# Kernel tuning notes

Measured on AMD Instinct MI355X. Metric: run time of the kernel, lower is better.

## Reference

```python
import jax, jax.numpy as jnp
import numpy as np

B, H, W, C = 4, 48, 48, 256
NUM_HEADS = 8
DEPTH = C // NUM_HEADS  # 32


def setup_inputs() -> dict:
    key = jax.random.key(0)
    ks = jax.random.split(key, 8)
    scale = 1.0 / np.sqrt(C)
    return {
        "inputs": jax.random.normal(ks[0], (B, H, W, C), dtype=jnp.float32),
        "wq": jax.random.normal(ks[1], (C, C), dtype=jnp.float32) * scale,
        "bq": jax.random.normal(ks[2], (C,), dtype=jnp.float32) * 0.01,
        "wk": jax.random.normal(ks[3], (C, C), dtype=jnp.float32) * scale,
        "bk": jax.random.normal(ks[4], (C,), dtype=jnp.float32) * 0.01,
        "wv": jax.random.normal(ks[5], (C, C), dtype=jnp.float32) * scale,
        "bv": jax.random.normal(ks[6], (C,), dtype=jnp.float32) * 0.01,
        "gamma": jax.random.normal(ks[7], (), dtype=jnp.float32) * 0.1,
    }


def reference(inputs, wq, bq, wk, bk, wv, bv, gamma):
    b, h, w, c = inputs.shape
    n = h * w  # number of tokens

    def proj_split(wm, bm):
        # 1x1 conv == per-pixel dense: [b,h,w,c] @ [c,c] + bias
        y = jnp.einsum('bhwc,cd->bhwd', inputs, wm) + bm
        # split heads -> [b, num_heads, n, depth]
        return y.reshape(b, n, NUM_HEADS, DEPTH).transpose(0, 2, 1, 3)

    q = proj_split(wq, bq) / jnp.sqrt(jnp.asarray(DEPTH, inputs.dtype))
    k = proj_split(wk, bk)
    v = proj_split(wv, bv)

    s = jnp.einsum('bnqd,bnkd->bnqk', q, k)        # [b, heads, n, n]
    a = jax.nn.softmax(s, axis=-1)
    o = jnp.einsum('bnqk,bnkd->bnqd', a, v)        # [b, heads, n, depth]
    o = o.transpose(0, 2, 1, 3).reshape(b, h, w, c)
    return gamma * o + inputs
```

## Files before the change

### kernel.cpp

```cpp
#include <hip/hip_runtime.h>
#include <hip/hip_bf16.h>
#include <cstdint>

#define B_    4
#define NH    8
#define N_TOK 2304
#define D_    32
#define C_    256
#define M_ROWS (B_ * N_TOK)
#define KVB   64
#define NT2   (N_TOK / KVB)
#define M_FIX 10.0f

typedef float  f32x4  __attribute__((ext_vector_type(4)));
typedef short  bf16x8 __attribute__((ext_vector_type(8)));

#define GLOADLDS(g, l) __builtin_amdgcn_global_load_lds( \
    (const __attribute__((address_space(1))) unsigned*)(g), \
    (__attribute__((address_space(3))) unsigned*)(l), 16, 0, 0)

static __device__ __forceinline__ unsigned short f2bf(float f) {
    union { float f; unsigned u; } v; v.f = f;
    unsigned u = v.u;
    u += 0x7FFF + ((u >> 16) & 1);
    return (unsigned short)(u >> 16);
}

static __device__ __forceinline__ unsigned cvt_pk_bf16(float a, float b) {
    unsigned r;
    asm("v_cvt_pk_bf16_f32 %0, %1, %2" : "=v"(r) : "v"(a), "v"(b));
    return r;
}

__global__ void k_prep(const float* __restrict__ x,
                       const float* __restrict__ w0, const float* __restrict__ w1,
                       const float* __restrict__ w2,
                       unsigned short* __restrict__ xb, unsigned short* __restrict__ wt) {
    __shared__ float tile[64][65];
    int bid = blockIdx.x;
    if (bid < 2304) {
        int i = bid * 256 + threadIdx.x;
        float4 v = reinterpret_cast<const float4*>(x)[i];
        ushort4 o;
        o.x = f2bf(v.x); o.y = f2bf(v.y); o.z = f2bf(v.z); o.w = f2bf(v.w);
        reinterpret_cast<ushort4*>(xb)[i] = o;
        return;
    }
    int t   = bid - 2304;
    int mat = t >> 4;  t &= 15;
    const float* w = (mat == 0) ? w0 : (mat == 1) ? w1 : w2;
    int tc  = (t & 3) * 64;
    int td  = (t >> 2) * 64;
    int tid = threadIdx.x;
    int r0  = tid >> 6;
    int x0  = tid & 63;
#pragma unroll
    for (int it = 0; it < 16; ++it) {
        int c = it * 4 + r0;
        tile[c][x0] = w[(tc + c) * C_ + td + x0];
    }
    __syncthreads();
    unsigned short* wto = wt + mat * (C_ * C_);
#pragma unroll
    for (int it = 0; it < 16; ++it) {
        int d = it * 4 + r0;
        wto[(td + d) * C_ + tc + x0] = f2bf(tile[x0][d]);
    }
}

__global__ __launch_bounds__(256) void k_proj(
    const unsigned short* __restrict__ xb,
    const unsigned short* __restrict__ wtb,
    const float* __restrict__ bq, const float* __restrict__ bk, const float* __restrict__ bv,
    unsigned short* __restrict__ qo, unsigned short* __restrict__ ko, unsigned short* __restrict__ vto)
{
    __shared__ __align__(16) unsigned short A_lds[3][64][32];
    __shared__ __align__(16) unsigned short B_lds[3][128][32];

    int rows0 = blockIdx.x * 64;
    int cols0 = blockIdx.y * 128;
    int mat   = cols0 >> 8;
    const float* bias = (mat == 0) ? bq : (mat == 1) ? bk : bv;
    float scale = (mat == 0) ? (0.17677669529663687f * 1.4426950408889634f) : 1.0f;

    int tid = threadIdx.x, wave = tid >> 6, lane = tid & 63;
    int lr = lane & 15, lg = lane >> 4;
    int wr = wave >> 1, wc = wave & 1;

    int srow = lane >> 2, sslot = lane & 3;
    int ra   = wave * 16 + srow;
    int keyA = ((ra >> 1) & 1) | (((ra >> 3) & 1) << 1);
    const unsigned short* asrc = xb + (rows0 + ra) * C_ + ((sslot ^ keyA) * 8);
    int rb   = wave * 32 + srow;
    int keyB0 = ((rb >> 1) & 1) | (((rb >> 3) & 1) << 1);
    int keyB1 = (((rb + 16) >> 1) & 1) | ((((rb + 16) >> 3) & 1) << 1);
    const unsigned short* bsrc0 = wtb + (cols0 + rb) * C_ + ((sslot ^ keyB0) * 8);
    const unsigned short* bsrc1 = wtb + (cols0 + rb + 16) * C_ + ((sslot ^ keyB1) * 8);

    char* aldsb = (char*)&A_lds[0][0][0];
    char* bldsb = (char*)&B_lds[0][0][0];
    int adst = wave * 1024;
    int bdst0 = wave * 2048, bdst1 = bdst0 + 1024;

    int xorb = (((lr >> 1) & 1) << 4) | (((lr >> 3) & 1) << 5);
    int fcol = (lg * 16) ^ xorb;
    int arow0 = wr * 32 + lr;
    int brow0 = wc * 64 + lr;

#define PSTAGE(ks, bidx) do {                               \
        int ko_ = (ks) * 32;                                \
        char* ad = aldsb + (bidx) * 4096;                   \
        char* bd = bldsb + (bidx) * 8192;                   \
        GLOADLDS(asrc + ko_, ad + adst);                    \
        GLOADLDS(bsrc0 + ko_, bd + bdst0);                  \
        GLOADLDS(bsrc1 + ko_, bd + bdst1);                  \
    } while (0)

    PSTAGE(0, 0);
    PSTAGE(1, 1);
    asm volatile("s_waitcnt vmcnt(3)" ::: "memory");
    __builtin_amdgcn_s_barrier();

    f32x4 acc[2][4];
#pragma unroll
    for (int i = 0; i < 2; ++i)
#pragma unroll
        for (int j = 0; j < 4; ++j) acc[i][j] = (f32x4){0.f, 0.f, 0.f, 0.f};

    int b0 = 0;
    for (int ks = 0; ks < 8; ++ks) {
        if (ks + 2 < 8) {
            int b2 = b0 + 2; if (b2 >= 3) b2 -= 3;
            PSTAGE(ks + 2, b2);
        }
        const char* ac = aldsb + b0 * 4096;
        const char* bc = bldsb + b0 * 8192;

        bf16x8 a[2], b[4];
#pragma unroll
        for (int fr = 0; fr < 2; ++fr)
            a[fr] = *reinterpret_cast<const bf16x8*>(ac + (arow0 + fr * 16) * 64 + fcol);
#pragma unroll
        for (int fn = 0; fn < 4; ++fn)
            b[fn] = *reinterpret_cast<const bf16x8*>(bc + (brow0 + fn * 16) * 64 + fcol);

        __builtin_amdgcn_s_setprio(1);
#pragma unroll
        for (int fr = 0; fr < 2; ++fr)
#pragma unroll
            for (int fn = 0; fn < 4; ++fn)
                acc[fr][fn] = __builtin_amdgcn_mfma_f32_16x16x32_bf16(a[fr], b[fn], acc[fr][fn], 0, 0, 0);
        __builtin_amdgcn_s_setprio(0);

        if (ks < 7) {
            if (ks + 2 < 8) asm volatile("s_waitcnt vmcnt(3)" ::: "memory");
            else            asm volatile("s_waitcnt vmcnt(0)" ::: "memory");
            __builtin_amdgcn_s_barrier();
        }
        b0 = (b0 + 1 == 3) ? 0 : b0 + 1;
    }
#undef PSTAGE

    int bidx = rows0 / N_TOK;
    int nb   = rows0 - bidx * N_TOK + wr * 32 + lg * 4;

    if (mat == 2) {
#pragma unroll
        for (int fr = 0; fr < 2; ++fr)
#pragma unroll
            for (int fn = 0; fn < 4; ++fn) {
                int cm = (cols0 & 255) + wc * 64 + fn * 16 + lr;
                float bsv = bias[cm];
                int hh = cm >> 5, d = cm & 31;
                uint2 pr;
                pr.x = cvt_pk_bf16(acc[fr][fn][0] + bsv, acc[fr][fn][1] + bsv);
                pr.y = cvt_pk_bf16(acc[fr][fn][2] + bsv, acc[fr][fn][3] + bsv);
                *reinterpret_cast<uint2*>(vto + ((bidx * NH + hh) * D_ + d) * N_TOK + nb + fr * 16) = pr;
            }
    } else {
        unsigned short* dst = (mat == 0) ? qo : ko;
#pragma unroll
        for (int fr = 0; fr < 2; ++fr)
#pragma unroll
            for (int fn = 0; fn < 4; ++fn) {
                int cm = (cols0 & 255) + wc * 64 + fn * 16 + lr;
                float bsv = bias[cm];
                int hh = cm >> 5, d = cm & 31;
#pragma unroll
                for (int j = 0; j < 4; ++j) {
                    float val = (acc[fr][fn][j] + bsv) * scale;
                    dst[((bidx * NH + hh) * N_TOK + nb + fr * 16 + j) * D_ + d] = f2bf(val);
                }
            }
    }
}

__global__ __launch_bounds__(256, 4) void k_attn(
    const unsigned short* __restrict__ qb,
    const unsigned short* __restrict__ kb,
    const unsigned short* __restrict__ vtg,
    const float* __restrict__ x,
    const float* __restrict__ gamma_p,
    float* __restrict__ out)
{
    __shared__ __align__(16) unsigned short K_lds[3][KVB][32];
    __shared__ __align__(16) unsigned short Vt_lds[3][32][KVB];

    int wid = (blockIdx.x & 7) * 72 + (blockIdx.x >> 3);
    int bh  = wid / 18;
    int qb0 = (wid % 18) * 128;

    int tid = threadIdx.x, wave = tid >> 6, lane = tid & 63;
    int lr = lane & 15, lg = lane >> 4;

    const unsigned short* Q  = qb  + bh * N_TOK * D_;
    const unsigned short* K  = kb  + bh * N_TOK * D_;
    const unsigned short* Vt = vtg + bh * D_ * N_TOK;

    int qrowA = qb0 + wave * 32 + lr;
    bf16x8 qA = *reinterpret_cast<const bf16x8*>(Q + qrowA * D_ + lg * 8);
    bf16x8 qB = *reinterpret_cast<const bf16x8*>(Q + (qrowA + 16) * D_ + lg * 8);

    bool stK = wave < 2;
    int kr0   = 32 * wave + (lane >> 2);
    int kslot = ((kr0 >> 1) & 1) | (((kr0 >> 3) & 1) << 1);
    int koff0 = kr0 * D_ + (((lane & 3) ^ kslot) * 8);
    int koff1 = koff0 + 16 * D_;
    int kdst0 = wave * 2048 + lane * 16;
    int kdst1 = kdst0 + 1024;
    int vw    = wave - 2;
    int vr0   = 16 * vw + (lane >> 3);
    int vkeyw = vr0 & 7;
    int voff0 = vr0 * N_TOK + (((lane & 7) ^ vkeyw) * 8);
    int voff1 = (vr0 + 8) * N_TOK + (((lane & 7) ^ vkeyw) * 8);
    int vdst0 = vw * 2048 + lane * 16;
    int vdst1 = vdst0 + 1024;

    char* kldsb = (char*)&K_lds[0][0][0];
    char* vldsb = (char*)&Vt_lds[0][0][0];

#define STAGE(st, bidx) do {                                    \
        if (stK) {                                              \
            const unsigned short* Kn = K + (st) * (KVB * D_);   \
            char* kd = kldsb + (bidx) * 4096;                   \
            GLOADLDS(Kn + koff0, kd + kdst0);                   \
            GLOADLDS(Kn + koff1, kd + kdst1);                   \
        } else {                                                \
            const unsigned short* Vn = Vt + (st) * KVB;         \
            char* vd = vldsb + (bidx) * 4096;                   \
            GLOADLDS(Vn + voff0, vd + vdst0);                   \
            GLOADLDS(Vn + voff1, vd + vdst1);                   \
        } } while (0)

    STAGE(0, 0);
    STAGE(1, 1);
    asm volatile("s_waitcnt vmcnt(2)" ::: "memory");
    __builtin_amdgcn_s_barrier();

    f32x4 accA0 = (f32x4){0.f, 0.f, 0.f, 0.f};
    f32x4 accA1 = (f32x4){0.f, 0.f, 0.f, 0.f};
    f32x4 accB0 = (f32x4){0.f, 0.f, 0.f, 0.f};
    f32x4 accB1 = (f32x4){0.f, 0.f, 0.f, 0.f};
    f32x4 acclA = (f32x4){0.f, 0.f, 0.f, 0.f};
    f32x4 acclB = (f32x4){0.f, 0.f, 0.f, 0.f};

    union { unsigned w[4]; bf16x8 v; } ones;
    ones.w[0] = 0x3F803F80u; ones.w[1] = 0x3F803F80u;
    ones.w[2] = 0x3F803F80u; ones.w[3] = 0x3F803F80u;

    int kread_key = (((lr >> 1) & 1) << 4) | (((lr >> 2) & 1) << 5);
    int krow_lane = (8 * (lr >> 2) + (lr & 3)) * 64 + ((lg * 16) ^ kread_key);
    int vkey = (lr & 7) << 4;

    const f32x4 zinit = (f32x4){-M_FIX, -M_FIX, -M_FIX, -M_FIX};

    int b0 = 0;
    for (int t = 0; t < NT2; ++t) {
        if (t + 2 < NT2) {
            int b2 = b0 + 2; if (b2 >= 3) b2 -= 3;
            STAGE(t + 2, b2);
        }
        const char* kc = kldsb + b0 * 4096;
        const char* vc = vldsb + b0 * 4096;

        f32x4 sA[4], sB[4];
        __builtin_amdgcn_s_setprio(1);
#pragma unroll
        for (int kt = 0; kt < 4; ++kt) {
            bf16x8 kf = *reinterpret_cast<const bf16x8*>(
                kc + (kt >> 1) * 2048 + (kt & 1) * 256 + krow_lane);
            sA[kt] = __builtin_amdgcn_mfma_f32_16x16x32_bf16(kf, qA, zinit, 0, 0, 0);
            sB[kt] = __builtin_amdgcn_mfma_f32_16x16x32_bf16(kf, qB, zinit, 0, 0, 0);
        }
        __builtin_amdgcn_s_setprio(0);

#pragma unroll
        for (int kseg = 0; kseg < 2; ++kseg) {
            union { unsigned w[4]; bf16x8 v; } paA, paB;
            paA.w[0] = cvt_pk_bf16(__builtin_amdgcn_exp2f(sA[2 * kseg][0]),
                                   __builtin_amdgcn_exp2f(sA[2 * kseg][1]));
            paA.w[1] = cvt_pk_bf16(__builtin_amdgcn_exp2f(sA[2 * kseg][2]),
                                   __builtin_amdgcn_exp2f(sA[2 * kseg][3]));
            paA.w[2] = cvt_pk_bf16(__builtin_amdgcn_exp2f(sA[2 * kseg + 1][0]),
                                   __builtin_amdgcn_exp2f(sA[2 * kseg + 1][1]));
            paA.w[3] = cvt_pk_bf16(__builtin_amdgcn_exp2f(sA[2 * kseg + 1][2]),
                                   __builtin_amdgcn_exp2f(sA[2 * kseg + 1][3]));
            paB.w[0] = cvt_pk_bf16(__builtin_amdgcn_exp2f(sB[2 * kseg][0]),
                                   __builtin_amdgcn_exp2f(sB[2 * kseg][1]));
            paB.w[1] = cvt_pk_bf16(__builtin_amdgcn_exp2f(sB[2 * kseg][2]),
                                   __builtin_amdgcn_exp2f(sB[2 * kseg][3]));
            paB.w[2] = cvt_pk_bf16(__builtin_amdgcn_exp2f(sB[2 * kseg + 1][0]),
                                   __builtin_amdgcn_exp2f(sB[2 * kseg + 1][1]));
            paB.w[3] = cvt_pk_bf16(__builtin_amdgcn_exp2f(sB[2 * kseg + 1][2]),
                                   __builtin_amdgcn_exp2f(sB[2 * kseg + 1][3]));
            int off = (kseg * 64 + lg * 16) ^ vkey;
            bf16x8 vf0 = *reinterpret_cast<const bf16x8*>(vc + lr * 128 + off);
            bf16x8 vf1 = *reinterpret_cast<const bf16x8*>(vc + (16 + lr) * 128 + off);
            accA0 = __builtin_amdgcn_mfma_f32_16x16x32_bf16(paA.v, vf0,    accA0, 0, 0, 0);
            accA1 = __builtin_amdgcn_mfma_f32_16x16x32_bf16(paA.v, vf1,    accA1, 0, 0, 0);
            accB0 = __builtin_amdgcn_mfma_f32_16x16x32_bf16(paB.v, vf0,    accB0, 0, 0, 0);
            accB1 = __builtin_amdgcn_mfma_f32_16x16x32_bf16(paB.v, vf1,    accB1, 0, 0, 0);
            acclA = __builtin_amdgcn_mfma_f32_16x16x32_bf16(paA.v, ones.v, acclA, 0, 0, 0);
            acclB = __builtin_amdgcn_mfma_f32_16x16x32_bf16(paB.v, ones.v, acclB, 0, 0, 0);
        }

        if (t < NT2 - 1) {
            if (t + 2 < NT2) asm volatile("s_waitcnt vmcnt(2)" ::: "memory");
            else             asm volatile("s_waitcnt vmcnt(0)" ::: "memory");
            __builtin_amdgcn_s_barrier();
        }
        b0 = (b0 + 1 == 3) ? 0 : b0 + 1;
    }
#undef STAGE

    float g = gamma_p[0];
    int b = bh >> 3, head = bh & 7;
#pragma unroll
    for (int j = 0; j < 4; ++j) {
        float linvA = 1.0f / acclA[j];
        float linvB = 1.0f / acclB[j];
        int nA = qb0 + wave * 32 + 4 * lg + j;
        long rA = (long)(b * N_TOK + nA) * C_ + head * 32;
        long rB = rA + 16L * C_;
        out[rA + lr]      = g * (accA0[j] * linvA) + x[rA + lr];
        out[rA + 16 + lr] = g * (accA1[j] * linvA) + x[rA + 16 + lr];
        out[rB + lr]      = g * (accB0[j] * linvB) + x[rB + lr];
        out[rB + 16 + lr] = g * (accB1[j] * linvB) + x[rB + 16 + lr];
    }
}

extern "C" void kernel_launch(void* const* d_in, const int* in_sizes, int n_in,
                              void* d_out, int out_size, void* d_ws, size_t ws_size,
                              hipStream_t stream) {
    const float* x     = (const float*)d_in[0];
    const float* wq    = (const float*)d_in[1];
    const float* bq    = (const float*)d_in[2];
    const float* wk    = (const float*)d_in[3];
    const float* bk    = (const float*)d_in[4];
    const float* wv    = (const float*)d_in[5];
    const float* bv    = (const float*)d_in[6];
    const float* gamma = (const float*)d_in[7];
    float* out = (float*)d_out;

    char* ws = (char*)d_ws;
    unsigned short* xb   = (unsigned short*)(ws);
    unsigned short* wt   = (unsigned short*)(ws + 4718592);
    unsigned short* qbuf = (unsigned short*)(ws + 5111808);
    unsigned short* kbuf = (unsigned short*)(ws + 9830400);
    unsigned short* vtg  = (unsigned short*)(ws + 14548992);

    k_prep<<<dim3(2352), dim3(256), 0, stream>>>(x, wq, wk, wv, xb, wt);
    k_proj<<<dim3(M_ROWS / 64, 6), dim3(256), 0, stream>>>(xb, wt, bq, bk, bv, qbuf, kbuf, vtg);
    k_attn<<<dim3(N_TOK / 128 * B_ * NH), dim3(256), 0, stream>>>(qbuf, kbuf, vtg, x, gamma, out);
}
```

Before: 58.50 us.

## Load K/V fragments directly from global into registers, dropping LDS staging

Replaces the triple-buffered global_load_lds staging of K and V tiles, along with its per-iteration waitcnt and barrier, with per-wave direct global loads into registers. K fragments are prefetched one iteration ahead and V fragments are loaded at the top of each iteration. This removes shared memory use and block-wide synchronisation, but each of the four waves now fetches the same K/V data separately, quadrupling global/L2 traffic, and V loads get less latency hiding. Launch bounds are lowered from 4 to 3 blocks per SIMD-level occupancy hint, giving more registers for the prefetch buffers.

```diff
diff --git a/kernel.cpp b/kernel.cpp
--- a/kernel.cpp
+++ b/kernel.cpp
@@ -195,7 +195,7 @@
     }
 }
 
-__global__ __launch_bounds__(256, 4) void k_attn(
+__global__ __launch_bounds__(256, 3) void k_attn(
     const unsigned short* __restrict__ qb,
     const unsigned short* __restrict__ kb,
     const unsigned short* __restrict__ vtg,
@@ -203,9 +203,6 @@
     const float* __restrict__ gamma_p,
     float* __restrict__ out)
 {
-    __shared__ __align__(16) unsigned short K_lds[3][KVB][32];
-    __shared__ __align__(16) unsigned short Vt_lds[3][32][KVB];
-
     int wid = (blockIdx.x & 7) * 72 + (blockIdx.x >> 3);
     int bh  = wid / 18;
     int qb0 = (wid % 18) * 128;
@@ -221,41 +218,17 @@
     bf16x8 qA = *reinterpret_cast<const bf16x8*>(Q + qrowA * D_ + lg * 8);
     bf16x8 qB = *reinterpret_cast<const bf16x8*>(Q + (qrowA + 16) * D_ + lg * 8);
 
-    bool stK = wave < 2;
-    int kr0   = 32 * wave + (lane >> 2);
-    int kslot = ((kr0 >> 1) & 1) | (((kr0 >> 3) & 1) << 1);
-    int koff0 = kr0 * D_ + (((lane & 3) ^ kslot) * 8);
-    int koff1 = koff0 + 16 * D_;
-    int kdst0 = wave * 2048 + lane * 16;
-    int kdst1 = kdst0 + 1024;
-    int vw    = wave - 2;
-    int vr0   = 16 * vw + (lane >> 3);
-    int vkeyw = vr0 & 7;
-    int voff0 = vr0 * N_TOK + (((lane & 7) ^ vkeyw) * 8);
-    int voff1 = (vr0 + 8) * N_TOK + (((lane & 7) ^ vkeyw) * 8);
-    int vdst0 = vw * 2048 + lane * 16;
-    int vdst1 = vdst0 + 1024;
-
-    char* kldsb = (char*)&K_lds[0][0][0];
-    char* vldsb = (char*)&Vt_lds[0][0][0];
-
-#define STAGE(st, bidx) do {                                    \
-        if (stK) {                                              \
-            const unsigned short* Kn = K + (st) * (KVB * D_);   \
-            char* kd = kldsb + (bidx) * 4096;                   \
-            GLOADLDS(Kn + koff0, kd + kdst0);                   \
-            GLOADLDS(Kn + koff1, kd + kdst1);                   \
-        } else {                                                \
-            const unsigned short* Vn = Vt + (st) * KVB;         \
-            char* vd = vldsb + (bidx) * 4096;                   \
-            GLOADLDS(Vn + voff0, vd + vdst0);                   \
-            GLOADLDS(Vn + voff1, vd + vdst1);                   \
-        } } while (0)
-
-    STAGE(0, 0);
-    STAGE(1, 1);
-    asm volatile("s_waitcnt vmcnt(2)" ::: "memory");
-    __builtin_amdgcn_s_barrier();
+    const unsigned short* K0 = K + (8 * (lr >> 2) + (lr & 3)) * D_ + lg * 8;
+    const unsigned short* V0 = Vt + lr * N_TOK + lg * 8;
+    const unsigned short* V1 = Vt + (16 + lr) * N_TOK + lg * 8;
+
+#define LDK(dst, t, kt) dst = *reinterpret_cast<const bf16x8*>( \
+        K0 + (t) * (KVB * D_) + (32 * ((kt) >> 1) + 4 * ((kt) & 1)) * D_)
+#define LDV(dst, t, kseg, half) dst = *reinterpret_cast<const bf16x8*>( \
+        ((half) ? V1 : V0) + (t) * KVB + (kseg) * 32)
+
+    bf16x8 kc0, kc1, kc2, kc3;
+    LDK(kc0, 0, 0); LDK(kc1, 0, 1); LDK(kc2, 0, 2); LDK(kc3, 0, 3);
 
     f32x4 accA0 = (f32x4){0.f, 0.f, 0.f, 0.f};
     f32x4 accA1 = (f32x4){0.f, 0.f, 0.f, 0.f};
@@ -268,30 +241,27 @@
     ones.w[0] = 0x3F803F80u; ones.w[1] = 0x3F803F80u;
     ones.w[2] = 0x3F803F80u; ones.w[3] = 0x3F803F80u;
 
-    int kread_key = (((lr >> 1) & 1) << 4) | (((lr >> 2) & 1) << 5);
-    int krow_lane = (8 * (lr >> 2) + (lr & 3)) * 64 + ((lg * 16) ^ kread_key);
-    int vkey = (lr & 7) << 4;
-
     const f32x4 zinit = (f32x4){-M_FIX, -M_FIX, -M_FIX, -M_FIX};
 
-    int b0 = 0;
     for (int t = 0; t < NT2; ++t) {
-        if (t + 2 < NT2) {
-            int b2 = b0 + 2; if (b2 >= 3) b2 -= 3;
-            STAGE(t + 2, b2);
+        bf16x8 vc0, vc1, vc2, vc3;
+        LDV(vc0, t, 0, 0); LDV(vc1, t, 0, 1); LDV(vc2, t, 1, 0); LDV(vc3, t, 1, 1);
+        bf16x8 kn0, kn1, kn2, kn3;
+        if (t + 1 < NT2) {
+            LDK(kn0, t + 1, 0); LDK(kn1, t + 1, 1);
+            LDK(kn2, t + 1, 2); LDK(kn3, t + 1, 3);
         }
-        const char* kc = kldsb + b0 * 4096;
-        const char* vc = vldsb + b0 * 4096;
 
         f32x4 sA[4], sB[4];
         __builtin_amdgcn_s_setprio(1);
-#pragma unroll
-        for (int kt = 0; kt < 4; ++kt) {
-            bf16x8 kf = *reinterpret_cast<const bf16x8*>(
-                kc + (kt >> 1) * 2048 + (kt & 1) * 256 + krow_lane);
-            sA[kt] = __builtin_amdgcn_mfma_f32_16x16x32_bf16(kf, qA, zinit, 0, 0, 0);
-            sB[kt] = __builtin_amdgcn_mfma_f32_16x16x32_bf16(kf, qB, zinit, 0, 0, 0);
-        }
+        sA[0] = __builtin_amdgcn_mfma_f32_16x16x32_bf16(kc0, qA, zinit, 0, 0, 0);
+        sB[0] = __builtin_amdgcn_mfma_f32_16x16x32_bf16(kc0, qB, zinit, 0, 0, 0);
+        sA[1] = __builtin_amdgcn_mfma_f32_16x16x32_bf16(kc1, qA, zinit, 0, 0, 0);
+        sB[1] = __builtin_amdgcn_mfma_f32_16x16x32_bf16(kc1, qB, zinit, 0, 0, 0);
+        sA[2] = __builtin_amdgcn_mfma_f32_16x16x32_bf16(kc2, qA, zinit, 0, 0, 0);
+        sB[2] = __builtin_amdgcn_mfma_f32_16x16x32_bf16(kc2, qB, zinit, 0, 0, 0);
+        sA[3] = __builtin_amdgcn_mfma_f32_16x16x32_bf16(kc3, qA, zinit, 0, 0, 0);
+        sB[3] = __builtin_amdgcn_mfma_f32_16x16x32_bf16(kc3, qB, zinit, 0, 0, 0);
         __builtin_amdgcn_s_setprio(0);
 
 #pragma unroll
@@ -313,9 +283,8 @@
                                    __builtin_amdgcn_exp2f(sB[2 * kseg + 1][1]));
             paB.w[3] = cvt_pk_bf16(__builtin_amdgcn_exp2f(sB[2 * kseg + 1][2]),
                                    __builtin_amdgcn_exp2f(sB[2 * kseg + 1][3]));
-            int off = (kseg * 64 + lg * 16) ^ vkey;
-            bf16x8 vf0 = *reinterpret_cast<const bf16x8*>(vc + lr * 128 + off);
-            bf16x8 vf1 = *reinterpret_cast<const bf16x8*>(vc + (16 + lr) * 128 + off);
+            bf16x8 vf0 = kseg ? vc2 : vc0;
+            bf16x8 vf1 = kseg ? vc3 : vc1;
             accA0 = __builtin_amdgcn_mfma_f32_16x16x32_bf16(paA.v, vf0,    accA0, 0, 0, 0);
             accA1 = __builtin_amdgcn_mfma_f32_16x16x32_bf16(paA.v, vf1,    accA1, 0, 0, 0);
             accB0 = __builtin_amdgcn_mfma_f32_16x16x32_bf16(paB.v, vf0,    accB0, 0, 0, 0);
@@ -324,14 +293,10 @@
             acclB = __builtin_amdgcn_mfma_f32_16x16x32_bf16(paB.v, ones.v, acclB, 0, 0, 0);
         }
 
-        if (t < NT2 - 1) {
-            if (t + 2 < NT2) asm volatile("s_waitcnt vmcnt(2)" ::: "memory");
-            else             asm volatile("s_waitcnt vmcnt(0)" ::: "memory");
-            __builtin_amdgcn_s_barrier();
-        }
-        b0 = (b0 + 1 == 3) ? 0 : b0 + 1;
-    }
-#undef STAGE
+        if (t + 1 < NT2) { kc0 = kn0; kc1 = kn1; kc2 = kn2; kc3 = kn3; }
+    }
+#undef LDK
+#undef LDV
 
     float g = gamma_p[0];
     int b = bh >> 3, head = bh & 7;
```

After: 98.47 us. 1.68x slower.

## Split attention KV range across two blocks and combine partials in a new kernel

Applied to the files above, without the earlier changes.

Splits the key/value sequence into two halves so each query tile is processed by two workgroups, doubling the grid from 576 to 1152 blocks to better fill the GPU's compute units. Because the softmax uses a fixed max offset, the partial numerators and denominators can simply be added. The first half writes fp32 partials into the output buffer, the second writes bf16 partials into the reused xb workspace, and row sums go to a new buffer. A separate combine kernel adds the partials, normalizes, and applies gamma plus the residual. This costs an extra launch, extra global traffic, and some precision loss from bf16 partials.

```diff
diff --git a/kernel.cpp b/kernel.cpp
--- a/kernel.cpp
+++ b/kernel.cpp
@@ -10,6 +10,8 @@
 #define M_ROWS (B_ * N_TOK)
 #define KVB   64
 #define NT2   (N_TOK / KVB)
+#define NSPLIT 2
+#define TILES_PER_SPLIT (NT2 / NSPLIT)
 #define M_FIX 10.0f
 
 typedef float  f32x4  __attribute__((ext_vector_type(4)));
@@ -199,16 +201,20 @@
     const unsigned short* __restrict__ qb,
     const unsigned short* __restrict__ kb,
     const unsigned short* __restrict__ vtg,
-    const float* __restrict__ x,
-    const float* __restrict__ gamma_p,
-    float* __restrict__ out)
+    float* __restrict__ opart,
+    unsigned short* __restrict__ obf,
+    float* __restrict__ lpart)
 {
     __shared__ __align__(16) unsigned short K_lds[3][KVB][32];
     __shared__ __align__(16) unsigned short Vt_lds[3][32][KVB];
 
-    int wid = (blockIdx.x & 7) * 72 + (blockIdx.x >> 3);
-    int bh  = wid / 18;
-    int qb0 = (wid % 18) * 128;
+    int wid = (blockIdx.x & 7) * 144 + (blockIdx.x >> 3);
+    int split = wid / 576;
+    int qid   = wid - split * 576;
+    int bh  = qid / 18;
+    int qb0 = (qid % 18) * 128;
+    int t0   = split * TILES_PER_SPLIT;
+    int tend = t0 + TILES_PER_SPLIT;
 
     int tid = threadIdx.x, wave = tid >> 6, lane = tid & 63;
     int lr = lane & 15, lg = lane >> 4;
@@ -252,8 +258,8 @@
             GLOADLDS(Vn + voff1, vd + vdst1);                   \
         } } while (0)
 
-    STAGE(0, 0);
-    STAGE(1, 1);
+    STAGE(t0, 0);
+    STAGE(t0 + 1, 1);
     asm volatile("s_waitcnt vmcnt(2)" ::: "memory");
     __builtin_amdgcn_s_barrier();
 
@@ -275,8 +281,8 @@
     const f32x4 zinit = (f32x4){-M_FIX, -M_FIX, -M_FIX, -M_FIX};
 
     int b0 = 0;
-    for (int t = 0; t < NT2; ++t) {
-        if (t + 2 < NT2) {
+    for (int t = t0; t < tend; ++t) {
+        if (t + 2 < tend) {
             int b2 = b0 + 2; if (b2 >= 3) b2 -= 3;
             STAGE(t + 2, b2);
         }
@@ -324,29 +330,56 @@
             acclB = __builtin_amdgcn_mfma_f32_16x16x32_bf16(paB.v, ones.v, acclB, 0, 0, 0);
         }
 
-        if (t < NT2 - 1) {
-            if (t + 2 < NT2) asm volatile("s_waitcnt vmcnt(2)" ::: "memory");
-            else             asm volatile("s_waitcnt vmcnt(0)" ::: "memory");
+        if (t < tend - 1) {
+            if (t + 2 < tend) asm volatile("s_waitcnt vmcnt(2)" ::: "memory");
+            else              asm volatile("s_waitcnt vmcnt(0)" ::: "memory");
             __builtin_amdgcn_s_barrier();
         }
         b0 = (b0 + 1 == 3) ? 0 : b0 + 1;
     }
 #undef STAGE
 
-    float g = gamma_p[0];
     int b = bh >> 3, head = bh & 7;
 #pragma unroll
     for (int j = 0; j < 4; ++j) {
-        float linvA = 1.0f / acclA[j];
-        float linvB = 1.0f / acclB[j];
         int nA = qb0 + wave * 32 + 4 * lg + j;
         long rA = (long)(b * N_TOK + nA) * C_ + head * 32;
         long rB = rA + 16L * C_;
-        out[rA + lr]      = g * (accA0[j] * linvA) + x[rA + lr];
-        out[rA + 16 + lr] = g * (accA1[j] * linvA) + x[rA + 16 + lr];
-        out[rB + lr]      = g * (accB0[j] * linvB) + x[rB + lr];
-        out[rB + 16 + lr] = g * (accB1[j] * linvB) + x[rB + 16 + lr];
-    }
+        if (split == 0) {
+            opart[rA + lr]      = accA0[j];
+            opart[rA + 16 + lr] = accA1[j];
+            opart[rB + lr]      = accB0[j];
+            opart[rB + 16 + lr] = accB1[j];
+        } else {
+            obf[rA + lr]      = f2bf(accA0[j]);
+            obf[rA + 16 + lr] = f2bf(accA1[j]);
+            obf[rB + lr]      = f2bf(accB0[j]);
+            obf[rB + 16 + lr] = f2bf(accB1[j]);
+        }
+        if (lr == 0) {
+            float* lp = lpart + split * (32 * N_TOK) + bh * N_TOK;
+            lp[nA]      = acclA[j];
+            lp[nA + 16] = acclB[j];
+        }
+    }
+}
+
+__global__ __launch_bounds__(256) void k_comb(
+    const unsigned short* __restrict__ obf,
+    const float* __restrict__ lpart,
+    const float* __restrict__ x,
+    const float* __restrict__ gamma_p,
+    float* __restrict__ out)
+{
+    int row = blockIdx.x;
+    int c   = threadIdx.x;
+    int b   = row / N_TOK, n = row - b * N_TOK;
+    int head = c >> 5;
+    int bh  = b * NH + head;
+    float l = lpart[bh * N_TOK + n] + lpart[32 * N_TOK + bh * N_TOK + n];
+    long i  = (long)row * C_ + c;
+    float O = out[i] + __uint_as_float(((unsigned)obf[i]) << 16);
+    out[i]  = gamma_p[0] * (O / l) + x[i];
 }
 
 extern "C" void kernel_launch(void* const* d_in, const int* in_sizes, int n_in,
@@ -368,8 +401,11 @@
     unsigned short* qbuf = (unsigned short*)(ws + 5111808);
     unsigned short* kbuf = (unsigned short*)(ws + 9830400);
     unsigned short* vtg  = (unsigned short*)(ws + 14548992);
+    float*          lpt  = (float*)(ws + 19267584);
 
     k_prep<<<dim3(2352), dim3(256), 0, stream>>>(x, wq, wk, wv, xb, wt);
     k_proj<<<dim3(M_ROWS / 64, 6), dim3(256), 0, stream>>>(xb, wt, bq, bk, bv, qbuf, kbuf, vtg);
-    k_attn<<<dim3(N_TOK / 128 * B_ * NH), dim3(256), 0, stream>>>(qbuf, kbuf, vtg, x, gamma, out);
-}
+    k_attn<<<dim3(N_TOK / 128 * B_ * NH * NSPLIT), dim3(256), 0, stream>>>(
+        qbuf, kbuf, vtg, out, xb, lpt);
+    k_comb<<<dim3(M_ROWS), dim3(256), 0, stream>>>(xb, lpt, x, gamma, out);
+}
```

Measured after the change: 61.82 us. 5.7% more time.
